# Performance work log

Measured on AMD Instinct MI355X. Metric: run time of the kernel, lower is better.

## Reference

```python
import jax, jax.numpy as jnp
import numpy as np

N = 100000
E = 1600000
IN_F = 128
OUT_F = 128
EPS = 1e-12


def setup_inputs() -> dict:
    key = jax.random.key(0)
    k1, k2, k3, k4, k5, k6 = jax.random.split(key, 6)
    x = jax.random.normal(k1, (N, IN_F), dtype=jnp.float32)
    rows = jnp.sort(jax.random.randint(k2, (E,), 0, N, dtype=jnp.int32))
    cols = jax.random.randint(k3, (E,), 0, N, dtype=jnp.int32)
    vals = jax.random.uniform(k4, (E,), dtype=jnp.float32)
    # nn.Linear(2*in_features, out_features): W is [out, 2*in], b is [out]
    bound = 1.0 / np.sqrt(2 * IN_F)
    W = jax.random.uniform(k5, (OUT_F, 2 * IN_F), dtype=jnp.float32, minval=-bound, maxval=bound)
    b = jax.random.uniform(k6, (OUT_F,), dtype=jnp.float32, minval=-bound, maxval=bound)
    return {"x": x, "rows": rows, "cols": cols, "vals": vals, "W": W, "b": b}


def reference(x, rows, cols, vals, W, b):
    # spmm(adj, x): gather source-node features, scale by edge weight,
    # segment-sum into destination rows.
    gathered = vals[:, None] * x[cols]                      # [E, in]
    neighbor = jax.ops.segment_sum(gathered, rows, num_segments=N)  # [N, in]
    combined = jnp.concatenate([x, neighbor], axis=1)       # [N, 2*in]
    out = combined @ W.T + b                                # [N, out]
    # F.normalize(out, p=2, dim=1): divide by max(||row||_2, eps)
    norm = jnp.sqrt(jnp.sum(out * out, axis=1, keepdims=True))
    return out / jnp.maximum(norm, EPS)
```

## Files before the change

kernel.cpp:

```cpp
#include <hip/hip_runtime.h>
#include <hip/hip_bf16.h>


typedef __bf16 bf16x8_t __attribute__((ext_vector_type(8)));
typedef float f32x4_t __attribute__((ext_vector_type(4)));
typedef float f32x2_t __attribute__((ext_vector_type(2)));
typedef unsigned int u32x4_t __attribute__((ext_vector_type(4)));

#define DESC_CAP 512
#define RING_D   8

__device__ __forceinline__ unsigned int f32_to_bf16(float f) {
    unsigned int u = __float_as_uint(f);
    unsigned int r = u + 0x7fffu + ((u >> 16) & 1u);
    return r >> 16;
}
__device__ __forceinline__ unsigned int pack2(float a, float b) {
    return f32_to_bf16(a) | (f32_to_bf16(b) << 16);
}
__device__ __forceinline__ float bflo(unsigned int p) { return __uint_as_float(p << 16); }
__device__ __forceinline__ float bfhi(unsigned int p) { return __uint_as_float(p & 0xffff0000u); }

__global__ void prep_kernel(const float* __restrict__ x, uint4* __restrict__ xb4,
                            const int* __restrict__ rows, int* __restrict__ row_ptr,
                            const float* __restrict__ W, uint4* __restrict__ Wf,
                            int Nn, int Ee, int xcast_blks, int rowptr_blks) {
    int blk = blockIdx.x;
    if (blk < xcast_blks) {
        int i = blk * 256 + threadIdx.x;
        if (i < Nn * 16) {
            const f32x4_t* xf = (const f32x4_t*)x;
            f32x4_t f0 = __builtin_nontemporal_load(&xf[(size_t)i * 2]);
            f32x4_t f1 = __builtin_nontemporal_load(&xf[(size_t)i * 2 + 1]);
            u32x4_t o;
            o.x = pack2(f0.x, f0.y); o.y = pack2(f0.z, f0.w);
            o.z = pack2(f1.x, f1.y); o.w = pack2(f1.z, f1.w);
            __builtin_nontemporal_store(o, (u32x4_t*)&xb4[i]);
        }
    } else if (blk < xcast_blks + rowptr_blks) {
        int n = (blk - xcast_blks) * 256 + threadIdx.x;
        if (n <= Nn) {
            int lo = 0, hi = Ee;
            while (lo < hi) {
                int mid = (lo + hi) >> 1;
                if (rows[mid] < n) lo = mid + 1; else hi = mid;
            }
            row_ptr[n] = lo;
        }
    } else {
        int i = (blk - xcast_blks - rowptr_blks) * 256 + threadIdx.x;
        int lane = i & 63, ks = (i >> 6) & 7, t = i >> 9;
        int row = t * 16 + (lane & 15);
        int col = ks * 32 + (lane >> 4) * 8;
        const float* p = W + (size_t)row * 256 + col;
        uint4 o;
        o.x = pack2(p[0], p[1]); o.y = pack2(p[2], p[3]);
        o.z = pack2(p[4], p[5]); o.w = pack2(p[6], p[7]);
        Wf[i] = o;
    }
}

__global__ void __launch_bounds__(256, 6)
fused_kernel(const int* __restrict__ row_ptr,
             const int* __restrict__ cols,
             const float* __restrict__ vals,
             const char* __restrict__ xbB,
             const bf16x8_t* __restrict__ Wf,
             const float* __restrict__ b,
             float* __restrict__ out, int Nn) {
    __shared__ int   rpS[17];
    __shared__ uint2 cvLDS[DESC_CAP];
    __shared__ uint4 nbLDS[16 * 17];
    __shared__ float __attribute__((aligned(16))) sqLDS[16][4];

    int lane = threadIdx.x & 63;
    int w    = threadIdx.x >> 6;
    int r0   = blockIdx.x * 16;

    if (threadIdx.x < 17)
        rpS[threadIdx.x] = row_ptr[min(r0 + (int)threadIdx.x, Nn)];
    __syncthreads();

    int eLo = rpS[0], eHi = rpS[16];
    int cnt = eHi - eLo;
    bool big = cnt > DESC_CAP;

    if (!big) {
        for (int i = threadIdx.x; i < cnt; i += 256) {
            int e = eLo + i;
            int c = __builtin_nontemporal_load(&cols[e]);
            float v = __builtin_nontemporal_load(&vals[e]);
            int d = (e >= rpS[8]) ? 8 : 0;
            d += (e >= rpS[d + 4]) ? 4 : 0;
            d += (e >= rpS[d + 2]) ? 2 : 0;
            d += (e >= rpS[d + 1]) ? 1 : 0;
            uint2 cv;
            cv.x = (unsigned)c | ((unsigned)d << 28);
            cv.y = __float_as_uint(v);
            cvLDS[i] = cv;
        }
    }
    {
        unsigned* nz = (unsigned*)nbLDS;
        for (int i = threadIdx.x; i < 16 * 17 * 4; i += 256) nz[i] = 0u;
    }
    __syncthreads();

    if (!big) {
        int wLo = __builtin_amdgcn_readfirstlane(rpS[w * 4]     - eLo);
        int wHi = __builtin_amdgcn_readfirstlane(rpS[w * 4 + 4] - eLo);
        int nEd = wHi - wLo;
        if (nEd > 0) {
            unsigned lane2 = (unsigned)lane << 2;
            int wHiM1 = wHi - 1;
            unsigned* nbW = (unsigned*)nbLDS;

            unsigned P[RING_D];
            uint2    cv[RING_D];
#pragma unroll
            for (int d = 0; d < RING_D; ++d) {
                int kd = min(wLo + d, wHiM1);
                cv[d] = cvLDS[kd];
                unsigned voff = ((cv[d].x & 0x0FFFFFFFu) << 8) | lane2;
                P[d] = *(const unsigned*)(xbB + voff);
            }
            int cur = (int)(cv[0].x >> 28);
            float ax = 0.f, ay = 0.f;

            int nit = (nEd + RING_D - 1) / RING_D;
            int k0 = wLo;
            for (int it = 0; it < nit; ++it, k0 += RING_D) {
#pragma unroll
                for (int d = 0; d < RING_D; ++d) {
                    int k = k0 + d;
                    uint2 cvk = cv[d];
                    int dk = (int)(cvk.x >> 28);
                    if (dk != cur) {
                        nbW[cur * 68 + lane] = pack2(ax, ay);
                        ax = 0.f; ay = 0.f;
                        cur = dk;
                    }
                    float vv = (k < wHi) ? __uint_as_float(cvk.y) : 0.f;
                    unsigned Pd = P[d];
                    ax += vv * bflo(Pd);
                    ay += vv * bfhi(Pd);
                    uint2 cvn = cvLDS[min(k + RING_D, wHiM1)];
                    unsigned voff = ((cvn.x & 0x0FFFFFFFu) << 8) | lane2;
                    P[d] = *(const unsigned*)(xbB + voff);
                    cv[d] = cvn;
                }
            }
            nbW[cur * 68 + lane] = pack2(ax, ay);
        }
    } else {
        int h = lane >> 4;
        int l = lane & 15;
        int node = w * 4 + h;
        int n = r0 + node;
        int nn = min(n, Nn - 1);
        int start = row_ptr[nn], end = row_ptr[nn + 1];
        if (n >= Nn) end = start;
        unsigned loff = (unsigned)l << 4;

        f32x2_t a0 = {0.f, 0.f}, a1 = {0.f, 0.f}, a2 = {0.f, 0.f}, a3 = {0.f, 0.f};

#define ACC1(p, V) {                                                        \
        f32x2_t vv2 = {(V), (V)};                                           \
        f32x2_t t0 = {bflo((p).x), bfhi((p).x)};                            \
        f32x2_t t1 = {bflo((p).y), bfhi((p).y)};                            \
        f32x2_t t2 = {bflo((p).z), bfhi((p).z)};                            \
        f32x2_t t3 = {bflo((p).w), bfhi((p).w)};                            \
        a0 += vv2 * t0; a1 += vv2 * t1; a2 += vv2 * t2; a3 += vv2 * t3;     \
}
#define EDGE4B(E, C0, C1, C2, C3, V0, V1, V2, V3)                               \
        {                                                                       \
            int q0 = min((E), end - 1),     q1 = min((E) + 1, end - 1);         \
            int q2 = min((E) + 2, end - 1), q3 = min((E) + 3, end - 1);         \
            C0 = cols[q0]; C1 = cols[q1]; C2 = cols[q2]; C3 = cols[q3];         \
            V0 = ((E)     < end) ? vals[q0] : 0.f;                              \
            V1 = ((E) + 1 < end) ? vals[q1] : 0.f;                              \
            V2 = ((E) + 2 < end) ? vals[q2] : 0.f;                              \
            V3 = ((E) + 3 < end) ? vals[q3] : 0.f;                              \
        }
        int e = start;
        int c0 = 0, c1 = 0, c2 = 0, c3 = 0;
        float v0 = 0.f, v1 = 0.f, v2 = 0.f, v3 = 0.f;
        if (e < end) EDGE4B(e, c0, c1, c2, c3, v0, v1, v2, v3);
        while (e < end) {
            int en = e + 4;
            int d0 = 0, d1 = 0, d2 = 0, d3 = 0;
            float w0 = 0.f, w1 = 0.f, w2 = 0.f, w3 = 0.f;
            if (en < end) EDGE4B(en, d0, d1, d2, d3, w0, w1, w2, w3);
            uint4 p0 = *(const uint4*)(xbB + (((unsigned)c0 << 8) | loff));
            uint4 p1 = *(const uint4*)(xbB + (((unsigned)c1 << 8) | loff));
            uint4 p2 = *(const uint4*)(xbB + (((unsigned)c2 << 8) | loff));
            uint4 p3 = *(const uint4*)(xbB + (((unsigned)c3 << 8) | loff));
            ACC1(p0, v0); ACC1(p1, v1); ACC1(p2, v2); ACC1(p3, v3);
            c0 = d0; c1 = d1; c2 = d2; c3 = d3;
            v0 = w0; v1 = w1; v2 = w2; v3 = w3;
            e = en;
        }
#undef EDGE4B
#undef ACC1
        uint4 o;
        o.x = pack2(a0.x, a0.y); o.y = pack2(a1.x, a1.y);
        o.z = pack2(a2.x, a2.y); o.w = pack2(a3.x, a3.y);
        nbLDS[node * 17 + l] = o;
    }
    __syncthreads();

    int m    = lane & 15;
    int quad = lane >> 4;

    int arow = min(r0 + m, Nn - 1);
    const bf16x8_t* Ax = (const bf16x8_t*)(xbB + (size_t)arow * 256);

    bf16x8_t a[8];
#pragma unroll
    for (int ks = 0; ks < 4; ++ks) a[ks] = Ax[ks * 4 + quad];
#pragma unroll
    for (int ks = 0; ks < 4; ++ks)
        a[4 + ks] = *(const bf16x8_t*)&nbLDS[m * 17 + ks * 4 + quad];

    f32x4_t acc[2];
    float bc[2];
#pragma unroll
    for (int j = 0; j < 2; ++j) {
        int t = w * 2 + j;
        acc[j] = (f32x4_t){0.f, 0.f, 0.f, 0.f};
        bc[j]  = b[t * 16 + m];
#pragma unroll
        for (int ks = 0; ks < 8; ++ks) {
            acc[j] = __builtin_amdgcn_mfma_f32_16x16x32_bf16(
                a[ks], Wf[(t * 8 + ks) * 64 + lane], acc[j], 0, 0, 0);
        }
    }

    float sq[4] = {0.f, 0.f, 0.f, 0.f};
#pragma unroll
    for (int j = 0; j < 2; ++j)
#pragma unroll
        for (int r = 0; r < 4; ++r) {
            float u = acc[j][r] + bc[j];
            sq[r] += u * u;
        }
#pragma unroll
    for (int off = 1; off <= 8; off <<= 1) {
#pragma unroll
        for (int r = 0; r < 4; ++r) sq[r] += __shfl_xor(sq[r], off, 64);
    }
    if (m == 0) {
#pragma unroll
        for (int r = 0; r < 4; ++r) sqLDS[quad * 4 + r][w] = sq[r];
    }
    __syncthreads();

    float scale[4];
#pragma unroll
    for (int r = 0; r < 4; ++r) {
        const float4 q4 = *(const float4*)sqLDS[quad * 4 + r];
        float tot = q4.x + q4.y + q4.z + q4.w;
        scale[r] = 1.f / fmaxf(sqrtf(tot), 1e-12f);
    }

#pragma unroll
    for (int r = 0; r < 4; ++r) {
        int row = r0 + quad * 4 + r;
        if (row < Nn) {
            float* orow = out + (size_t)row * 128;
#pragma unroll
            for (int j = 0; j < 2; ++j) {
                int t = w * 2 + j;
                __builtin_nontemporal_store((acc[j][r] + bc[j]) * scale[r],
                                            &orow[t * 16 + m]);
            }
        }
    }
}

extern "C" void kernel_launch(void* const* d_in, const int* in_sizes, int n_in,
                              void* d_out, int out_size, void* d_ws, size_t ws_size,
                              hipStream_t stream) {
    const float* x    = (const float*)d_in[0];
    const int*   rows = (const int*)  d_in[1];
    const int*   cols = (const int*)  d_in[2];
    const float* vals = (const float*)d_in[3];
    const float* W    = (const float*)d_in[4];
    const float* b    = (const float*)d_in[5];
    float*       out  = (float*)d_out;

    const int Nn = in_sizes[0] / 128;
    const int Ee = in_sizes[1];

    char*  ws      = (char*)d_ws;
    int*   row_ptr = (int*)ws;
    uint4* Wf      = (uint4*)(ws + 448 * 1024);
    uint4* xb      = (uint4*)(ws + 640 * 1024);

    const int xcast_blks  = (Nn * 16 + 255) / 256;
    const int rowptr_blks = (Nn + 1 + 255) / 256;
    const int wcast_blks  = 16;

    prep_kernel<<<xcast_blks + rowptr_blks + wcast_blks, 256, 0, stream>>>(
        x, xb, rows, row_ptr, W, Wf, Nn, Ee, xcast_blks, rowptr_blks);
    fused_kernel<<<(Nn + 15) / 16, 256, 0, stream>>>(
        row_ptr, cols, vals, (const char*)xb,
        (const bf16x8_t*)Wf, b, out, Nn);
}
```

Before: 194.7 us.

## Quantize gathered node features to per-row int8 with scale folded into edge weights

Replaces the bf16 copy of x used for the neighbor gather with an int8 copy plus a per-row float scale. The scale is multiplied into each edge value when descriptors are staged, and the self-feature operand of the MFMA is now read from fp32 x and converted to bf16 in the fused kernel. This halves the bytes fetched per gathered row and shrinks the prep write, but adds a scale lookup per edge, sign-extension work, and coarser precision for the aggregated features. The large-row fallback path also drops its 4-edge prefetch unrolling for a simple loop.

Result: slower. 202.1 us (+3.8%).

```diff
diff --git a/kernel.cpp b/kernel.cpp
--- a/kernel.cpp
+++ b/kernel.cpp
@@ -5,7 +5,7 @@
 typedef __bf16 bf16x8_t __attribute__((ext_vector_type(8)));
 typedef float f32x4_t __attribute__((ext_vector_type(4)));
 typedef float f32x2_t __attribute__((ext_vector_type(2)));
-typedef unsigned int u32x4_t __attribute__((ext_vector_type(4)));
+typedef unsigned int u32x2_t __attribute__((ext_vector_type(2)));
 
 #define DESC_CAP 512
 #define RING_D   8
@@ -18,24 +18,42 @@
 __device__ __forceinline__ unsigned int pack2(float a, float b) {
     return f32_to_bf16(a) | (f32_to_bf16(b) << 16);
 }
-__device__ __forceinline__ float bflo(unsigned int p) { return __uint_as_float(p << 16); }
-__device__ __forceinline__ float bfhi(unsigned int p) { return __uint_as_float(p & 0xffff0000u); }
-
-__global__ void prep_kernel(const float* __restrict__ x, uint4* __restrict__ xb4,
+
+__global__ void prep_kernel(const float* __restrict__ x, u32x2_t* __restrict__ xq,
+                            float* __restrict__ xs,
                             const int* __restrict__ rows, int* __restrict__ row_ptr,
                             const float* __restrict__ W, uint4* __restrict__ Wf,
                             int Nn, int Ee, int xcast_blks, int rowptr_blks) {
     int blk = blockIdx.x;
     if (blk < xcast_blks) {
-        int i = blk * 256 + threadIdx.x;
-        if (i < Nn * 16) {
-            const f32x4_t* xf = (const f32x4_t*)x;
-            f32x4_t f0 = __builtin_nontemporal_load(&xf[(size_t)i * 2]);
-            f32x4_t f1 = __builtin_nontemporal_load(&xf[(size_t)i * 2 + 1]);
-            u32x4_t o;
-            o.x = pack2(f0.x, f0.y); o.y = pack2(f0.z, f0.w);
-            o.z = pack2(f1.x, f1.y); o.w = pack2(f1.z, f1.w);
-            __builtin_nontemporal_store(o, (u32x4_t*)&xb4[i]);
+        int lane = threadIdx.x & 63;
+        int wv   = threadIdx.x >> 6;
+        int r    = blk * 16 + wv * 4 + (lane >> 4);
+        int fc   = (lane & 15) * 8;
+        if (r < Nn) {
+            const f32x4_t* pf = (const f32x4_t*)(x + (size_t)r * 128 + fc);
+            f32x4_t f0 = __builtin_nontemporal_load(pf);
+            f32x4_t f1 = __builtin_nontemporal_load(pf + 1);
+            float m = fmaxf(fmaxf(fmaxf(fabsf(f0.x), fabsf(f0.y)),
+                                  fmaxf(fabsf(f0.z), fabsf(f0.w))),
+                            fmaxf(fmaxf(fabsf(f1.x), fabsf(f1.y)),
+                                  fmaxf(fabsf(f1.z), fabsf(f1.w))));
+            m = fmaxf(m, __shfl_xor(m, 1, 64));
+            m = fmaxf(m, __shfl_xor(m, 2, 64));
+            m = fmaxf(m, __shfl_xor(m, 4, 64));
+            m = fmaxf(m, __shfl_xor(m, 8, 64));
+            float inv = (m > 0.f) ? 127.f / m : 0.f;
+            int q0 = (int)rintf(f0.x * inv), q1 = (int)rintf(f0.y * inv);
+            int q2 = (int)rintf(f0.z * inv), q3 = (int)rintf(f0.w * inv);
+            int q4 = (int)rintf(f1.x * inv), q5 = (int)rintf(f1.y * inv);
+            int q6 = (int)rintf(f1.z * inv), q7 = (int)rintf(f1.w * inv);
+            u32x2_t o;
+            o.x = (q0 & 255) | ((q1 & 255) << 8) | ((q2 & 255) << 16)
+                | ((unsigned)(q3 & 255) << 24);
+            o.y = (q4 & 255) | ((q5 & 255) << 8) | ((q6 & 255) << 16)
+                | ((unsigned)(q7 & 255) << 24);
+            __builtin_nontemporal_store(o, &xq[(size_t)r * 16 + (lane & 15)]);
+            if ((lane & 15) == 0) xs[r] = m * (1.f / 127.f);
         }
     } else if (blk < xcast_blks + rowptr_blks) {
         int n = (blk - xcast_blks) * 256 + threadIdx.x;
@@ -64,7 +82,9 @@
 fused_kernel(const int* __restrict__ row_ptr,
              const int* __restrict__ cols,
              const float* __restrict__ vals,
-             const char* __restrict__ xbB,
+             const float* __restrict__ x,
+             const float* __restrict__ xs,
+             const char* __restrict__ xqB,
              const bf16x8_t* __restrict__ Wf,
              const float* __restrict__ b,
              float* __restrict__ out, int Nn) {
@@ -90,13 +110,14 @@
             int e = eLo + i;
             int c = __builtin_nontemporal_load(&cols[e]);
             float v = __builtin_nontemporal_load(&vals[e]);
+            float vw = v * xs[c];
             int d = (e >= rpS[8]) ? 8 : 0;
             d += (e >= rpS[d + 4]) ? 4 : 0;
             d += (e >= rpS[d + 2]) ? 2 : 0;
             d += (e >= rpS[d + 1]) ? 1 : 0;
             uint2 cv;
             cv.x = (unsigned)c | ((unsigned)d << 28);
-            cv.y = __float_as_uint(v);
+            cv.y = __float_as_uint(vw);
             cvLDS[i] = cv;
         }
     }
@@ -111,7 +132,7 @@
         int wHi = __builtin_amdgcn_readfirstlane(rpS[w * 4 + 4] - eLo);
         int nEd = wHi - wLo;
         if (nEd > 0) {
-            unsigned lane2 = (unsigned)lane << 2;
+            unsigned lane2 = (unsigned)lane << 1;
             int wHiM1 = wHi - 1;
             unsigned* nbW = (unsigned*)nbLDS;
 
@@ -121,8 +142,8 @@
             for (int d = 0; d < RING_D; ++d) {
                 int kd = min(wLo + d, wHiM1);
                 cv[d] = cvLDS[kd];
-                unsigned voff = ((cv[d].x & 0x0FFFFFFFu) << 8) | lane2;
-                P[d] = *(const unsigned*)(xbB + voff);
+                unsigned voff = ((cv[d].x & 0x0FFFFFFFu) << 7) | lane2;
+                P[d] = *(const unsigned short*)(xqB + voff);
             }
             int cur = (int)(cv[0].x >> 28);
             float ax = 0.f, ay = 0.f;
@@ -142,11 +163,13 @@
                     }
                     float vv = (k < wHi) ? __uint_as_float(cvk.y) : 0.f;
                     unsigned Pd = P[d];
-                    ax += vv * bflo(Pd);
-                    ay += vv * bfhi(Pd);
+                    float fx = (float)(int)(signed char)(Pd & 0xffu);
+                    float fy = (float)(int)(signed char)((Pd >> 8) & 0xffu);
+                    ax += vv * fx;
+                    ay += vv * fy;
                     uint2 cvn = cvLDS[min(k + RING_D, wHiM1)];
-                    unsigned voff = ((cvn.x & 0x0FFFFFFFu) << 8) | lane2;
-                    P[d] = *(const unsigned*)(xbB + voff);
+                    unsigned voff = ((cvn.x & 0x0FFFFFFFu) << 7) | lane2;
+                    P[d] = *(const unsigned short*)(xqB + voff);
                     cv[d] = cvn;
                 }
             }
@@ -160,48 +183,22 @@
         int nn = min(n, Nn - 1);
         int start = row_ptr[nn], end = row_ptr[nn + 1];
         if (n >= Nn) end = start;
-        unsigned loff = (unsigned)l << 4;
+        unsigned loff = (unsigned)l << 3;
 
         f32x2_t a0 = {0.f, 0.f}, a1 = {0.f, 0.f}, a2 = {0.f, 0.f}, a3 = {0.f, 0.f};
-
-#define ACC1(p, V) {                                                        \
-        f32x2_t vv2 = {(V), (V)};                                           \
-        f32x2_t t0 = {bflo((p).x), bfhi((p).x)};                            \
-        f32x2_t t1 = {bflo((p).y), bfhi((p).y)};                            \
-        f32x2_t t2 = {bflo((p).z), bfhi((p).z)};                            \
-        f32x2_t t3 = {bflo((p).w), bfhi((p).w)};                            \
-        a0 += vv2 * t0; a1 += vv2 * t1; a2 += vv2 * t2; a3 += vv2 * t3;     \
-}
-#define EDGE4B(E, C0, C1, C2, C3, V0, V1, V2, V3)                               \
-        {                                                                       \
-            int q0 = min((E), end - 1),     q1 = min((E) + 1, end - 1);         \
-            int q2 = min((E) + 2, end - 1), q3 = min((E) + 3, end - 1);         \
-            C0 = cols[q0]; C1 = cols[q1]; C2 = cols[q2]; C3 = cols[q3];         \
-            V0 = ((E)     < end) ? vals[q0] : 0.f;                              \
-            V1 = ((E) + 1 < end) ? vals[q1] : 0.f;                              \
-            V2 = ((E) + 2 < end) ? vals[q2] : 0.f;                              \
-            V3 = ((E) + 3 < end) ? vals[q3] : 0.f;                              \
-        }
-        int e = start;
-        int c0 = 0, c1 = 0, c2 = 0, c3 = 0;
-        float v0 = 0.f, v1 = 0.f, v2 = 0.f, v3 = 0.f;
-        if (e < end) EDGE4B(e, c0, c1, c2, c3, v0, v1, v2, v3);
-        while (e < end) {
-            int en = e + 4;
-            int d0 = 0, d1 = 0, d2 = 0, d3 = 0;
-            float w0 = 0.f, w1 = 0.f, w2 = 0.f, w3 = 0.f;
-            if (en < end) EDGE4B(en, d0, d1, d2, d3, w0, w1, w2, w3);
-            uint4 p0 = *(const uint4*)(xbB + (((unsigned)c0 << 8) | loff));
-            uint4 p1 = *(const uint4*)(xbB + (((unsigned)c1 << 8) | loff));
-            uint4 p2 = *(const uint4*)(xbB + (((unsigned)c2 << 8) | loff));
-            uint4 p3 = *(const uint4*)(xbB + (((unsigned)c3 << 8) | loff));
-            ACC1(p0, v0); ACC1(p1, v1); ACC1(p2, v2); ACC1(p3, v3);
-            c0 = d0; c1 = d1; c2 = d2; c3 = d3;
-            v0 = w0; v1 = w1; v2 = w2; v3 = w3;
-            e = en;
-        }
-#undef EDGE4B
-#undef ACC1
+        for (int e = start; e < end; ++e) {
+            int   c = cols[e];
+            float v = vals[e] * xs[c];
+            uint2 p = *(const uint2*)(xqB + (((unsigned)c << 7) | loff));
+            a0.x += v * (float)(int)(signed char)(p.x & 0xffu);
+            a0.y += v * (float)(int)(signed char)((p.x >> 8) & 0xffu);
+            a1.x += v * (float)(int)(signed char)((p.x >> 16) & 0xffu);
+            a1.y += v * (float)(int)(signed char)(p.x >> 24);
+            a2.x += v * (float)(int)(signed char)(p.y & 0xffu);
+            a2.y += v * (float)(int)(signed char)((p.y >> 8) & 0xffu);
+            a3.x += v * (float)(int)(signed char)((p.y >> 16) & 0xffu);
+            a3.y += v * (float)(int)(signed char)(p.y >> 24);
+        }
         uint4 o;
         o.x = pack2(a0.x, a0.y); o.y = pack2(a1.x, a1.y);
         o.z = pack2(a2.x, a2.y); o.w = pack2(a3.x, a3.y);
@@ -213,11 +210,19 @@
     int quad = lane >> 4;
 
     int arow = min(r0 + m, Nn - 1);
-    const bf16x8_t* Ax = (const bf16x8_t*)(xbB + (size_t)arow * 256);
+    const float* xrow = x + (size_t)arow * 128;
 
     bf16x8_t a[8];
 #pragma unroll
-    for (int ks = 0; ks < 4; ++ks) a[ks] = Ax[ks * 4 + quad];
+    for (int ks = 0; ks < 4; ++ks) {
+        const f32x4_t* pf = (const f32x4_t*)(xrow + 32 * ks + 8 * quad);
+        f32x4_t f0 = pf[0];
+        f32x4_t f1 = pf[1];
+        union { bf16x8_t v; unsigned u[4]; } au;
+        au.u[0] = pack2(f0.x, f0.y); au.u[1] = pack2(f0.z, f0.w);
+        au.u[2] = pack2(f1.x, f1.y); au.u[3] = pack2(f1.z, f1.w);
+        a[ks] = au.v;
+    }
 #pragma unroll
     for (int ks = 0; ks < 4; ++ks)
         a[4 + ks] = *(const bf16x8_t*)&nbLDS[m * 17 + ks * 4 + quad];
@@ -292,18 +297,19 @@
     const int Nn = in_sizes[0] / 128;
     const int Ee = in_sizes[1];
 
-    char*  ws      = (char*)d_ws;
-    int*   row_ptr = (int*)ws;
-    uint4* Wf      = (uint4*)(ws + 448 * 1024);
-    uint4* xb      = (uint4*)(ws + 640 * 1024);
-
-    const int xcast_blks  = (Nn * 16 + 255) / 256;
+    char*    ws      = (char*)d_ws;
+    int*     row_ptr = (int*)ws;
+    uint4*   Wf      = (uint4*)(ws + 448 * 1024);
+    float*   xs      = (float*)(ws + 512 * 1024);
+    u32x2_t* xq      = (u32x2_t*)(ws + 1024 * 1024);
+
+    const int xcast_blks  = (Nn + 15) / 16;
     const int rowptr_blks = (Nn + 1 + 255) / 256;
     const int wcast_blks  = 16;
 
     prep_kernel<<<xcast_blks + rowptr_blks + wcast_blks, 256, 0, stream>>>(
-        x, xb, rows, row_ptr, W, Wf, Nn, Ee, xcast_blks, rowptr_blks);
+        x, xq, xs, rows, row_ptr, W, Wf, Nn, Ee, xcast_blks, rowptr_blks);
     fused_kernel<<<(Nn + 15) / 16, 256, 0, stream>>>(
-        row_ptr, cols, vals, (const char*)xb,
+        row_ptr, cols, vals, x, xs, (const char*)xq,
         (const bf16x8_t*)Wf, b, out, Nn);
 }
```

## Split fused SpMM+GEMM kernel into separate aggregation and GEMM kernels

Applied to the files above, without the earlier changes.

Splits the single kernel into an aggregation kernel that writes bf16 neighbor sums to a global workspace buffer and a separate GEMM+normalize kernel that reads them back. The fused kernel is kept as a fallback when the workspace is too small. The aim is to let each phase run at its own occupancy, without the MFMA register pressure limiting the gather phase. The cost is an extra global round trip of the neighbor tensor and one more launch. The large-row gather path is also simplified from a 4-edge prefetched loop to a plain per-edge loop.

After: 222.3 us. +14.1%, slower.

```diff
diff --git a/kernel.cpp b/kernel.cpp
--- a/kernel.cpp
+++ b/kernel.cpp
@@ -60,18 +60,15 @@
     }
 }
 
-__global__ void __launch_bounds__(256, 6)
-fused_kernel(const int* __restrict__ row_ptr,
-             const int* __restrict__ cols,
-             const float* __restrict__ vals,
-             const char* __restrict__ xbB,
-             const bf16x8_t* __restrict__ Wf,
-             const float* __restrict__ b,
-             float* __restrict__ out, int Nn) {
+__global__ void __launch_bounds__(256)
+agg_kernel(const int* __restrict__ row_ptr,
+           const int* __restrict__ cols,
+           const float* __restrict__ vals,
+           const char* __restrict__ xbB,
+           uint4* __restrict__ nbG, int Nn) {
     __shared__ int   rpS[17];
     __shared__ uint2 cvLDS[DESC_CAP];
     __shared__ uint4 nbLDS[16 * 17];
-    __shared__ float __attribute__((aligned(16))) sqLDS[16][4];
 
     int lane = threadIdx.x & 63;
     int w    = threadIdx.x >> 6;
@@ -163,45 +160,17 @@
         unsigned loff = (unsigned)l << 4;
 
         f32x2_t a0 = {0.f, 0.f}, a1 = {0.f, 0.f}, a2 = {0.f, 0.f}, a3 = {0.f, 0.f};
-
-#define ACC1(p, V) {                                                        \
-        f32x2_t vv2 = {(V), (V)};                                           \
-        f32x2_t t0 = {bflo((p).x), bfhi((p).x)};                            \
-        f32x2_t t1 = {bflo((p).y), bfhi((p).y)};                            \
-        f32x2_t t2 = {bflo((p).z), bfhi((p).z)};                            \
-        f32x2_t t3 = {bflo((p).w), bfhi((p).w)};                            \
-        a0 += vv2 * t0; a1 += vv2 * t1; a2 += vv2 * t2; a3 += vv2 * t3;     \
-}
-#define EDGE4B(E, C0, C1, C2, C3, V0, V1, V2, V3)                               \
-        {                                                                       \
-            int q0 = min((E), end - 1),     q1 = min((E) + 1, end - 1);         \
-            int q2 = min((E) + 2, end - 1), q3 = min((E) + 3, end - 1);         \
-            C0 = cols[q0]; C1 = cols[q1]; C2 = cols[q2]; C3 = cols[q3];         \
-            V0 = ((E)     < end) ? vals[q0] : 0.f;                              \
-            V1 = ((E) + 1 < end) ? vals[q1] : 0.f;                              \
-            V2 = ((E) + 2 < end) ? vals[q2] : 0.f;                              \
-            V3 = ((E) + 3 < end) ? vals[q3] : 0.f;                              \
-        }
-        int e = start;
-        int c0 = 0, c1 = 0, c2 = 0, c3 = 0;
-        float v0 = 0.f, v1 = 0.f, v2 = 0.f, v3 = 0.f;
-        if (e < end) EDGE4B(e, c0, c1, c2, c3, v0, v1, v2, v3);
-        while (e < end) {
-            int en = e + 4;
-            int d0 = 0, d1 = 0, d2 = 0, d3 = 0;
-            float w0 = 0.f, w1 = 0.f, w2 = 0.f, w3 = 0.f;
-            if (en < end) EDGE4B(en, d0, d1, d2, d3, w0, w1, w2, w3);
-            uint4 p0 = *(const uint4*)(xbB + (((unsigned)c0 << 8) | loff));
-            uint4 p1 = *(const uint4*)(xbB + (((unsigned)c1 << 8) | loff));
-            uint4 p2 = *(const uint4*)(xbB + (((unsigned)c2 << 8) | loff));
-            uint4 p3 = *(const uint4*)(xbB + (((unsigned)c3 << 8) | loff));
-            ACC1(p0, v0); ACC1(p1, v1); ACC1(p2, v2); ACC1(p3, v3);
-            c0 = d0; c1 = d1; c2 = d2; c3 = d3;
-            v0 = w0; v1 = w1; v2 = w2; v3 = w3;
-            e = en;
-        }
-#undef EDGE4B
-#undef ACC1
+        for (int e = start; e < end; ++e) {
+            int   c = cols[e];
+            float v = vals[e];
+            uint4 p = *(const uint4*)(xbB + (((unsigned)c << 8) | loff));
+            f32x2_t vv = {v, v};
+            f32x2_t t0 = {bflo(p.x), bfhi(p.x)};
+            f32x2_t t1 = {bflo(p.y), bfhi(p.y)};
+            f32x2_t t2 = {bflo(p.z), bfhi(p.z)};
+            f32x2_t t3 = {bflo(p.w), bfhi(p.w)};
+            a0 += vv * t0; a1 += vv * t1; a2 += vv * t2; a3 += vv * t3;
+        }
         uint4 o;
         o.x = pack2(a0.x, a0.y); o.y = pack2(a1.x, a1.y);
         o.z = pack2(a2.x, a2.y); o.w = pack2(a3.x, a3.y);
@@ -209,18 +178,40 @@
     }
     __syncthreads();
 
+    {
+        int row = threadIdx.x >> 4;
+        int l   = threadIdx.x & 15;
+        if (r0 + row < Nn) {
+            u32x4_t val = *(const u32x4_t*)&nbLDS[row * 17 + l];
+            __builtin_nontemporal_store(
+                val, (u32x4_t*)&nbG[(size_t)(r0 + row) * 16 + l]);
+        }
+    }
+}
+
+__global__ void __launch_bounds__(256)
+gemm_kernel(const char* __restrict__ xbB,
+            const char* __restrict__ nbB,
+            const bf16x8_t* __restrict__ Wf,
+            const float* __restrict__ b,
+            float* __restrict__ out, int Nn) {
+    __shared__ float __attribute__((aligned(16))) sqLDS[16][4];
+
+    int lane = threadIdx.x & 63;
+    int w    = threadIdx.x >> 6;
     int m    = lane & 15;
     int quad = lane >> 4;
+    int r0   = blockIdx.x * 16;
 
     int arow = min(r0 + m, Nn - 1);
     const bf16x8_t* Ax = (const bf16x8_t*)(xbB + (size_t)arow * 256);
+    const bf16x8_t* Nx = (const bf16x8_t*)(nbB + (size_t)arow * 256);
 
     bf16x8_t a[8];
 #pragma unroll
     for (int ks = 0; ks < 4; ++ks) a[ks] = Ax[ks * 4 + quad];
 #pragma unroll
-    for (int ks = 0; ks < 4; ++ks)
-        a[4 + ks] = *(const bf16x8_t*)&nbLDS[m * 17 + ks * 4 + quad];
+    for (int ks = 0; ks < 4; ++ks) a[4 + ks] = Nx[ks * 4 + quad];
 
     f32x4_t acc[2];
     float bc[2];
@@ -263,6 +254,191 @@
         scale[r] = 1.f / fmaxf(sqrtf(tot), 1e-12f);
     }
 
+#pragma unroll
+    for (int r = 0; r < 4; ++r) {
+        int row = r0 + quad * 4 + r;
+        if (row < Nn) {
+            float* orow = out + (size_t)row * 128;
+#pragma unroll
+            for (int j = 0; j < 2; ++j) {
+                int t = w * 2 + j;
+                __builtin_nontemporal_store((acc[j][r] + bc[j]) * scale[r],
+                                            &orow[t * 16 + m]);
+            }
+        }
+    }
+}
+
+__global__ void __launch_bounds__(256, 6)
+fused_kernel(const int* __restrict__ row_ptr,
+             const int* __restrict__ cols,
+             const float* __restrict__ vals,
+             const char* __restrict__ xbB,
+             const bf16x8_t* __restrict__ Wf,
+             const float* __restrict__ b,
+             float* __restrict__ out, int Nn) {
+    __shared__ int   rpS[17];
+    __shared__ uint2 cvLDS[DESC_CAP];
+    __shared__ uint4 nbLDS[16 * 17];
+    __shared__ float __attribute__((aligned(16))) sqLDS[16][4];
+
+    int lane = threadIdx.x & 63;
+    int w    = threadIdx.x >> 6;
+    int r0   = blockIdx.x * 16;
+
+    if (threadIdx.x < 17)
+        rpS[threadIdx.x] = row_ptr[min(r0 + (int)threadIdx.x, Nn)];
+    __syncthreads();
+
+    int eLo = rpS[0], eHi = rpS[16];
+    int cnt = eHi - eLo;
+    bool big = cnt > DESC_CAP;
+
+    if (!big) {
+        for (int i = threadIdx.x; i < cnt; i += 256) {
+            int e = eLo + i;
+            int c = __builtin_nontemporal_load(&cols[e]);
+            float v = __builtin_nontemporal_load(&vals[e]);
+            int d = (e >= rpS[8]) ? 8 : 0;
+            d += (e >= rpS[d + 4]) ? 4 : 0;
+            d += (e >= rpS[d + 2]) ? 2 : 0;
+            d += (e >= rpS[d + 1]) ? 1 : 0;
+            uint2 cv;
+            cv.x = (unsigned)c | ((unsigned)d << 28);
+            cv.y = __float_as_uint(v);
+            cvLDS[i] = cv;
+        }
+    }
+    {
+        unsigned* nz = (unsigned*)nbLDS;
+        for (int i = threadIdx.x; i < 16 * 17 * 4; i += 256) nz[i] = 0u;
+    }
+    __syncthreads();
+
+    if (!big) {
+        int wLo = __builtin_amdgcn_readfirstlane(rpS[w * 4]     - eLo);
+        int wHi = __builtin_amdgcn_readfirstlane(rpS[w * 4 + 4] - eLo);
+        int nEd = wHi - wLo;
+        if (nEd > 0) {
+            unsigned lane2 = (unsigned)lane << 2;
+            int wHiM1 = wHi - 1;
+            unsigned* nbW = (unsigned*)nbLDS;
+            unsigned P[RING_D];
+            uint2    cv[RING_D];
+#pragma unroll
+            for (int d = 0; d < RING_D; ++d) {
+                int kd = min(wLo + d, wHiM1);
+                cv[d] = cvLDS[kd];
+                unsigned voff = ((cv[d].x & 0x0FFFFFFFu) << 8) | lane2;
+                P[d] = *(const unsigned*)(xbB + voff);
+            }
+            int cur = (int)(cv[0].x >> 28);
+            float ax = 0.f, ay = 0.f;
+            int nit = (nEd + RING_D - 1) / RING_D;
+            int k0 = wLo;
+            for (int it = 0; it < nit; ++it, k0 += RING_D) {
+#pragma unroll
+                for (int d = 0; d < RING_D; ++d) {
+                    int k = k0 + d;
+                    uint2 cvk = cv[d];
+                    int dk = (int)(cvk.x >> 28);
+                    if (dk != cur) {
+                        nbW[cur * 68 + lane] = pack2(ax, ay);
+                        ax = 0.f; ay = 0.f;
+                        cur = dk;
+                    }
+                    float vv = (k < wHi) ? __uint_as_float(cvk.y) : 0.f;
+                    unsigned Pd = P[d];
+                    ax += vv * bflo(Pd);
+                    ay += vv * bfhi(Pd);
+                    uint2 cvn = cvLDS[min(k + RING_D, wHiM1)];
+                    unsigned voff = ((cvn.x & 0x0FFFFFFFu) << 8) | lane2;
+                    P[d] = *(const unsigned*)(xbB + voff);
+                    cv[d] = cvn;
+                }
+            }
+            nbW[cur * 68 + lane] = pack2(ax, ay);
+        }
+    } else {
+        int h = lane >> 4;
+        int l = lane & 15;
+        int node = w * 4 + h;
+        int n = r0 + node;
+        int nn = min(n, Nn - 1);
+        int start = row_ptr[nn], end = row_ptr[nn + 1];
+        if (n >= Nn) end = start;
+        unsigned loff = (unsigned)l << 4;
+        f32x2_t a0 = {0.f, 0.f}, a1 = {0.f, 0.f}, a2 = {0.f, 0.f}, a3 = {0.f, 0.f};
+        for (int e = start; e < end; ++e) {
+            int   c = cols[e];
+            float v = vals[e];
+            uint4 p = *(const uint4*)(xbB + (((unsigned)c << 8) | loff));
+            f32x2_t vv = {v, v};
+            f32x2_t t0 = {bflo(p.x), bfhi(p.x)};
+            f32x2_t t1 = {bflo(p.y), bfhi(p.y)};
+            f32x2_t t2 = {bflo(p.z), bfhi(p.z)};
+            f32x2_t t3 = {bflo(p.w), bfhi(p.w)};
+            a0 += vv * t0; a1 += vv * t1; a2 += vv * t2; a3 += vv * t3;
+        }
+        uint4 o;
+        o.x = pack2(a0.x, a0.y); o.y = pack2(a1.x, a1.y);
+        o.z = pack2(a2.x, a2.y); o.w = pack2(a3.x, a3.y);
+        nbLDS[node * 17 + l] = o;
+    }
+    __syncthreads();
+
+    int m    = lane & 15;
+    int quad = lane >> 4;
+    int arow = min(r0 + m, Nn - 1);
+    const bf16x8_t* Ax = (const bf16x8_t*)(xbB + (size_t)arow * 256);
+
+    bf16x8_t a[8];
+#pragma unroll
+    for (int ks = 0; ks < 4; ++ks) a[ks] = Ax[ks * 4 + quad];
+#pragma unroll
+    for (int ks = 0; ks < 4; ++ks)
+        a[4 + ks] = *(const bf16x8_t*)&nbLDS[m * 17 + ks * 4 + quad];
+
+    f32x4_t acc[2];
+    float bc[2];
+#pragma unroll
+    for (int j = 0; j < 2; ++j) {
+        int t = w * 2 + j;
+        acc[j] = (f32x4_t){0.f, 0.f, 0.f, 0.f};
+        bc[j]  = b[t * 16 + m];
+#pragma unroll
+        for (int ks = 0; ks < 8; ++ks) {
+            acc[j] = __builtin_amdgcn_mfma_f32_16x16x32_bf16(
+                a[ks], Wf[(t * 8 + ks) * 64 + lane], acc[j], 0, 0, 0);
+        }
+    }
+
+    float sq[4] = {0.f, 0.f, 0.f, 0.f};
+#pragma unroll
+    for (int j = 0; j < 2; ++j)
+#pragma unroll
+        for (int r = 0; r < 4; ++r) {
+            float u = acc[j][r] + bc[j];
+            sq[r] += u * u;
+        }
+#pragma unroll
+    for (int off = 1; off <= 8; off <<= 1) {
+#pragma unroll
+        for (int r = 0; r < 4; ++r) sq[r] += __shfl_xor(sq[r], off, 64);
+    }
+    if (m == 0) {
+#pragma unroll
+        for (int r = 0; r < 4; ++r) sqLDS[quad * 4 + r][w] = sq[r];
+    }
+    __syncthreads();
+
+    float scale[4];
+#pragma unroll
+    for (int r = 0; r < 4; ++r) {
+        const float4 q4 = *(const float4*)sqLDS[quad * 4 + r];
+        float tot = q4.x + q4.y + q4.z + q4.w;
+        scale[r] = 1.f / fmaxf(sqrtf(tot), 1e-12f);
+    }
 #pragma unroll
     for (int r = 0; r < 4; ++r) {
         int row = r0 + quad * 4 + r;
@@ -296,14 +472,26 @@
     int*   row_ptr = (int*)ws;
     uint4* Wf      = (uint4*)(ws + 448 * 1024);
     uint4* xb      = (uint4*)(ws + 640 * 1024);
+    size_t nb_off  = 640 * 1024 + (size_t)Nn * 256;
+    uint4* nb      = (uint4*)(ws + nb_off);
+    size_t need    = nb_off + (size_t)Nn * 256;
 
     const int xcast_blks  = (Nn * 16 + 255) / 256;
     const int rowptr_blks = (Nn + 1 + 255) / 256;
     const int wcast_blks  = 16;
+    const int grid        = (Nn + 15) / 16;
 
     prep_kernel<<<xcast_blks + rowptr_blks + wcast_blks, 256, 0, stream>>>(
         x, xb, rows, row_ptr, W, Wf, Nn, Ee, xcast_blks, rowptr_blks);
-    fused_kernel<<<(Nn + 15) / 16, 256, 0, stream>>>(
-        row_ptr, cols, vals, (const char*)xb,
-        (const bf16x8_t*)Wf, b, out, Nn);
-}
+
+    if (ws_size >= need) {
+        agg_kernel<<<grid, 256, 0, stream>>>(
+            row_ptr, cols, vals, (const char*)xb, nb, Nn);
+        gemm_kernel<<<grid, 256, 0, stream>>>(
+            (const char*)xb, (const char*)nb, (const bf16x8_t*)Wf, b, out, Nn);
+    } else {
+        fused_kernel<<<grid, 256, 0, stream>>>(
+            row_ptr, cols, vals, (const char*)xb,
+            (const bf16x8_t*)Wf, b, out, Nn);
+    }
+}
```
